# Kernel optimization log

Hardware: AMD Instinct MI355X
Metric: run time of the kernel (lower is better)

Reference implementation:

```python
import jax, jax.numpy as jnp
import numpy as np

N = 100000
E = 1600000
NFEAT = 256
NHID = 128
LATENT = 64


def setup_inputs() -> dict:
    key = jax.random.key(0)
    ks = jax.random.split(key, 12)
    x = jax.random.normal(ks[0], (N, NFEAT), dtype=jnp.float32)
    edge_index = jax.random.randint(ks[1], (2, E), 0, N, dtype=jnp.int32)
    edge_weight = jax.random.uniform(ks[2], (E,), dtype=jnp.float32)
    # GraphConvolution params: uniform(-stdv, stdv), stdv = 1/sqrt(out_features)
    s1 = 1.0 / np.sqrt(NHID)
    gc1_w = jax.random.uniform(ks[3], (NFEAT, NHID), minval=-s1, maxval=s1, dtype=jnp.float32)
    gc1_b = jax.random.uniform(ks[4], (NHID,), minval=-s1, maxval=s1, dtype=jnp.float32)
    gc2_w = jax.random.uniform(ks[5], (NHID, NHID), minval=-s1, maxval=s1, dtype=jnp.float32)
    gc2_b = jax.random.uniform(ks[6], (NHID,), minval=-s1, maxval=s1, dtype=jnp.float32)
    # nn.Linear default init: uniform(-1/sqrt(fan_in), 1/sqrt(fan_in))
    s2 = 1.0 / np.sqrt(NHID)
    mu_w = jax.random.uniform(ks[7], (NHID, LATENT), minval=-s2, maxval=s2, dtype=jnp.float32)
    mu_b = jax.random.uniform(ks[8], (LATENT,), minval=-s2, maxval=s2, dtype=jnp.float32)
    lv_w = jax.random.uniform(ks[9], (NHID, LATENT), minval=-s2, maxval=s2, dtype=jnp.float32)
    lv_b = jax.random.uniform(ks[10], (LATENT,), minval=-s2, maxval=s2, dtype=jnp.float32)
    return {"x": x, "edge_index": edge_index, "edge_weight": edge_weight,
            "gc1_w": gc1_w, "gc1_b": gc1_b, "gc2_w": gc2_w, "gc2_b": gc2_b,
            "mu_w": mu_w, "mu_b": mu_b, "lv_w": lv_w, "lv_b": lv_b}


def _spmm(edge_index, edge_weight, support):
    # out[row] += w * support[col]  (sparse adj @ dense support)
    row, col = edge_index[0], edge_index[1]
    msgs = support[col] * edge_weight[:, None]          # [E, F]
    return jax.ops.segment_sum(msgs, row, num_segments=N)


def reference(x, edge_index, edge_weight, gc1_w, gc1_b, gc2_w, gc2_b,
              mu_w, mu_b, lv_w, lv_b):
    # gc1: mm -> spmm -> bias -> relu (dropout is identity in eval mode)
    h = jax.nn.relu(_spmm(edge_index, edge_weight, x @ gc1_w) + gc1_b)
    h = jax.nn.relu(_spmm(edge_index, edge_weight, h @ gc2_w) + gc2_b)
    mu = h @ mu_w + mu_b
    log_var = h @ lv_w + lv_b
    return mu, log_var
```

## Files before the change

### kernel.cpp

```cpp
#include <hip/hip_runtime.h>
#include <hip/hip_fp16.h>

#define N_NODES 100000
#define N_EDGES 1600000
#define NFEAT   256
#define NHID    128
#define LATENT  64

#define NBUCKET 782
#define NBLKH   196
#define CHUNK   8192
#define NHIST   (NBUCKET * NBLKH)
#define NROWT   196
#define NHISTT  300

typedef __attribute__((ext_vector_type(8))) short s16x8;
typedef __attribute__((ext_vector_type(4))) float f32x4;

__device__ __forceinline__ unsigned short f2bf(float f) {
    union { float f; unsigned u; } v; v.f = f;
    unsigned r = v.u + 0x7fffu + ((v.u >> 16) & 1u);
    return (unsigned short)(r >> 16);
}
__device__ __forceinline__ float bf2f(unsigned short s) {
    union { unsigned u; float f; } v; v.u = ((unsigned)s) << 16;
    return v.f;
}
__device__ __forceinline__ float w15_decode(unsigned pv) {
    return __half2float(__ushort_as_half((unsigned short)(pv & 0x7fffu)));
}

__device__ __forceinline__ int incl_scan512(int v, int t, int (&s)[2][512]) {
    s[0][t] = v;
    __syncthreads();
    int p = 0;
    for (int off = 1; off < 512; off <<= 1) {
        int x = s[p][t];
        if (t >= off) x += s[p][t - off];
        s[p ^ 1][t] = x;
        p ^= 1;
        __syncthreads();
    }
    return s[p][t];
}


__device__ __forceinline__ void prep_body(
    int c, int K, int Ntot, int ncol0, int ldb0, int ldb1,
    const float* __restrict__ B0, const float* __restrict__ B1,
    unsigned short* __restrict__ out)
{
    int K8 = K >> 3;
    int total = (Ntot >> 4) * K8 * 16;
    if (c >= total) return;
    int m  = c & 15;
    int kc = (c >> 4) % K8;
    int nt = (c >> 4) / K8;
    int col = nt * 16 + m;
    const float* src; int ld, cc;
    if (col < ncol0) { src = B0; ld = ldb0; cc = col; }
    else             { src = B1; ld = ldb1; cc = col - ncol0; }
    s16x8 v;
    #pragma unroll
    for (int j = 0; j < 8; ++j)
        v[j] = (short)f2bf(src[(size_t)(kc * 8 + j) * ld + cc]);
    *(s16x8*)&out[(size_t)c * 8] = v;
}


__global__ __launch_bounds__(256) void k_pre(
    const int* __restrict__ rows, int* __restrict__ deg,
    int* __restrict__ histG,
    const float* __restrict__ gc1_w, unsigned short* __restrict__ w1p,
    const float* __restrict__ gc2_w, unsigned short* __restrict__ w2p,
    const float* __restrict__ mu_w, const float* __restrict__ lv_w,
    unsigned short* __restrict__ w3p)
{
    int b = blockIdx.x;
    int t = threadIdx.x;
    if (b < NBLKH) {
        __shared__ int hist[NBUCKET];
        for (int i = t; i < NBUCKET; i += 256) hist[i] = 0;
        __syncthreads();
        int base = b * CHUNK;
        #pragma unroll 4
        for (int i = 0; i < CHUNK / 256; ++i) {
            int e = base + i * 256 + t;
            if (e < N_EDGES) {
                int r = rows[e];
                atomicAdd(&deg[r], 1);
                atomicAdd(&hist[r >> 7], 1);
            }
        }
        __syncthreads();
        for (int i = t; i < NBUCKET; i += 256)
            histG[(size_t)i * NBLKH + b] = hist[i];
    } else if (b < NBLKH + 16) {
        prep_body((b - NBLKH) * 256 + t, NFEAT, NHID, NHID, NHID, NHID, gc1_w, gc1_w, w1p);
    } else if (b < NBLKH + 24) {
        prep_body((b - NBLKH - 16) * 256 + t, NHID, NHID, NHID, NHID, NHID, gc2_w, gc2_w, w2p);
    } else {
        prep_body((b - NBLKH - 24) * 256 + t, NHID, NHID, LATENT, LATENT, LATENT, mu_w, lv_w, w3p);
    }
}


__global__ __launch_bounds__(512) void k_scanA(
    const int* __restrict__ deg, int* __restrict__ row_excl, int* __restrict__ rbsum,
    const int* __restrict__ histG, int* __restrict__ hist_excl, int* __restrict__ hbsum)
{
    __shared__ int s[2][512];
    int b = blockIdx.x, t = threadIdx.x;
    if (b < NROWT) {
        int i = b * 512 + t;
        int v = (i < N_NODES) ? deg[i] : 0;
        int incl = incl_scan512(v, t, s);
        if (i < N_NODES) row_excl[i] = incl - v;
        if (t == 511) rbsum[b] = incl;
    } else {
        int bb = b - NROWT;
        int i = bb * 512 + t;
        int v = (i < NHIST) ? histG[i] : 0;
        int incl = incl_scan512(v, t, s);
        if (i < NHIST) hist_excl[i] = incl - v;
        if (t == 511) hbsum[bb] = incl;
    }
}

__global__ __launch_bounds__(512) void k_scanB(int* __restrict__ rbsum,
                                               int* __restrict__ hbsum)
{
    __shared__ int s[2][512];
    int t = threadIdx.x;
    int* arr = (blockIdx.x == 0) ? rbsum : hbsum;
    int n    = (blockIdx.x == 0) ? NROWT : NHISTT;
    int v = (t < n) ? arr[t] : 0;
    int incl = incl_scan512(v, t, s);
    if (t < n) arr[t] = incl - v;
}

__global__ __launch_bounds__(512) void k_scanC(
    const int* __restrict__ row_excl, const int* __restrict__ rbsum,
    int* __restrict__ row_ptr,
    const int* __restrict__ hist_excl, const int* __restrict__ hbsum,
    int* __restrict__ scanned)
{
    int b = blockIdx.x, t = threadIdx.x;
    if (b < NROWT) {
        int i = b * 512 + t;
        if (i < N_NODES) row_ptr[i] = row_excl[i] + rbsum[b];
        if (b == 0 && t == 0) row_ptr[N_NODES] = N_EDGES;
    } else {
        int bb = b - NROWT;
        int i = bb * 512 + t;
        if (i < NHIST) scanned[i] = hist_excl[i] + hbsum[bb];
    }
}


__global__ __launch_bounds__(256) void k_scatterA(
    const int* __restrict__ rows, const int* __restrict__ cols,
    const float* __restrict__ ew, const int* __restrict__ scanned,
    uint2* __restrict__ tmp)
{
    __shared__ int cur[NBUCKET];
    int b = blockIdx.x, t = threadIdx.x;
    for (int i = t; i < NBUCKET; i += 256)
        cur[i] = scanned[(size_t)i * NBLKH + b];
    __syncthreads();
    int base = b * CHUNK;
    #pragma unroll 4
    for (int i = 0; i < CHUNK / 256; ++i) {
        int e = base + i * 256 + t;
        if (e < N_EDGES) {
            int r = rows[e];
            unsigned hv = (unsigned)__half_as_ushort(__float2half(ew[e]));
            unsigned pv = ((unsigned)cols[e] << 15) | (hv & 0x7fffu);
            int p = atomicAdd(&cur[r >> 7], 1);
            tmp[p] = make_uint2(pv, (unsigned)r);
        }
    }
}


__global__ __launch_bounds__(256) void k_passB(
    const int* __restrict__ row_ptr, const uint2* __restrict__ tmp,
    unsigned* __restrict__ ecw)
{
    __shared__ int cur[128];
    int b  = blockIdx.x;
    int r0 = b * 128;
    int t  = threadIdx.x;
    if (t < 128) {
        int rr = r0 + t;
        cur[t] = (rr < N_NODES) ? row_ptr[rr] : N_EDGES;
    }
    __syncthreads();
    int beg = row_ptr[r0];
    int rend = r0 + 128; if (rend > N_NODES) rend = N_NODES;
    int end = row_ptr[rend];
    for (int e = beg + t; e < end; e += 256) {
        uint2 v = tmp[e];
        int p = atomicAdd(&cur[v.y & 127], 1);
        ecw[p] = v.x;
    }
}


template<int AMODE, int OMODE>
__global__ __launch_bounds__(256) void k_gemm(
    int K, const float* __restrict__ A32, const unsigned short* __restrict__ A16,
    const unsigned short* __restrict__ Bpre,
    unsigned short* __restrict__ C16,
    float* __restrict__ C0, float* __restrict__ C1,
    const float* __restrict__ bias0, const float* __restrict__ bias1)
{
    __shared__ unsigned short As[2048];
    __shared__ unsigned short Bs[8192];

    const int t    = threadIdx.x;
    const int m0   = blockIdx.x * 32;
    const int lane = t & 63;
    const int w    = t >> 6;
    const int rt   = w & 1;
    const int ntb  = (w >> 1) * 4;
    const int fm   = lane & 15;
    const int q    = lane >> 4;
    const int K8   = K >> 3;

    f32x4 acc[4] = {};

    for (int kt = 0; kt < K; kt += 64) {
        {
            int r = t >> 3, kc = t & 7;
            int lo = ((r >> 4) * 8 + kc) * 128 + (r & 15) * 8;
            if (AMODE == 0) {
                const float* g = A32 + (size_t)(m0 + r) * K + kt + kc * 8;
                float4 a = *(const float4*)g;
                float4 b = *(const float4*)(g + 4);
                s16x8 v;
                v[0] = (short)f2bf(a.x); v[1] = (short)f2bf(a.y);
                v[2] = (short)f2bf(a.z); v[3] = (short)f2bf(a.w);
                v[4] = (short)f2bf(b.x); v[5] = (short)f2bf(b.y);
                v[6] = (short)f2bf(b.z); v[7] = (short)f2bf(b.w);
                *(s16x8*)&As[lo] = v;
            } else {
                const unsigned short* g = A16 + (size_t)(m0 + r) * 128 + kt + kc * 8;
                *(s16x8*)&As[lo] = *(const s16x8*)g;
            }
        }
        {
            int ktc = kt >> 3;
            #pragma unroll
            for (int i = 0; i < 4; ++i) {
                int c  = t + i * 256;
                int nt = c >> 7, kc = (c >> 4) & 7, m = c & 15;
                const unsigned short* g =
                    Bpre + ((size_t)(nt * K8 + ktc + kc) * 16 + m) * 8;
                *(s16x8*)&Bs[c * 8] = *(const s16x8*)g;
            }
        }
        __syncthreads();
        #pragma unroll
        for (int kk = 0; kk < 2; ++kk) {
            int kcq = kk * 4 + q;
            s16x8 a = *(const s16x8*)&As[(rt * 8 + kcq) * 128 + fm * 8];
            #pragma unroll
            for (int i = 0; i < 4; ++i) {
                s16x8 b = *(const s16x8*)&Bs[((ntb + i) * 8 + kcq) * 128 + fm * 8];
                acc[i] = __builtin_amdgcn_mfma_f32_16x16x32_bf16(a, b, acc[i], 0, 0, 0);
            }
        }
        __syncthreads();
    }

    #pragma unroll
    for (int i = 0; i < 4; ++i) {
        int col = (ntb + i) * 16 + fm;
        #pragma unroll
        for (int j = 0; j < 4; ++j) {
            int r = m0 + rt * 16 + q * 4 + j;
            float v = acc[i][j];
            if (OMODE == 0) {
                C16[(size_t)r * 128 + col] = f2bf(v);
            } else {
                if (col < 64) C0[(size_t)r * 64 + col]      = v + bias0[col];
                else          C1[(size_t)r * 64 + col - 64] = v + bias1[col - 64];
            }
        }
    }
}


__global__ __launch_bounds__(256) void k_spmm(const int* __restrict__ row_ptr,
                                              const unsigned* __restrict__ ecw,
                                              const unsigned short* __restrict__ sup,
                                              const float* __restrict__ bias,
                                              unsigned short* __restrict__ out) {
    int wave = threadIdx.x >> 6;
    int lane = threadIdx.x & 63;
    int row  = blockIdx.x * 4 + wave;
    if (row >= N_NODES) return;
    int half = lane >> 5;
    int fl   = lane & 31;

    int beg = row_ptr[row];
    int end = row_ptr[row + 1];
    float a0 = 0.f, a1 = 0.f, a2 = 0.f, a3 = 0.f;

    int n8 = beg + ((end - beg) & ~7);
    for (int e = beg; e < n8; e += 8) {
        unsigned q0 = ecw[e + 0 + half];
        unsigned q1 = ecw[e + 2 + half];
        unsigned q2 = ecw[e + 4 + half];
        unsigned q3 = ecw[e + 6 + half];
        uint2 v0 = *(const uint2*)(sup + (size_t)(q0 >> 15) * NHID + fl * 4);
        uint2 v1 = *(const uint2*)(sup + (size_t)(q1 >> 15) * NHID + fl * 4);
        uint2 v2 = *(const uint2*)(sup + (size_t)(q2 >> 15) * NHID + fl * 4);
        uint2 v3 = *(const uint2*)(sup + (size_t)(q3 >> 15) * NHID + fl * 4);
        float w0 = w15_decode(q0), w1 = w15_decode(q1);
        float w2 = w15_decode(q2), w3 = w15_decode(q3);
        a0 += w0 * bf2f((unsigned short)v0.x);
        a1 += w0 * bf2f((unsigned short)(v0.x >> 16));
        a2 += w0 * bf2f((unsigned short)v0.y);
        a3 += w0 * bf2f((unsigned short)(v0.y >> 16));
        a0 += w1 * bf2f((unsigned short)v1.x);
        a1 += w1 * bf2f((unsigned short)(v1.x >> 16));
        a2 += w1 * bf2f((unsigned short)v1.y);
        a3 += w1 * bf2f((unsigned short)(v1.y >> 16));
        a0 += w2 * bf2f((unsigned short)v2.x);
        a1 += w2 * bf2f((unsigned short)(v2.x >> 16));
        a2 += w2 * bf2f((unsigned short)v2.y);
        a3 += w2 * bf2f((unsigned short)(v2.y >> 16));
        a0 += w3 * bf2f((unsigned short)v3.x);
        a1 += w3 * bf2f((unsigned short)(v3.x >> 16));
        a2 += w3 * bf2f((unsigned short)v3.y);
        a3 += w3 * bf2f((unsigned short)(v3.y >> 16));
    }
    for (int e = n8; e < end; e += 2) {
        int ee = e + half;
        if (ee < end) {
            unsigned q = ecw[ee];
            uint2 v = *(const uint2*)(sup + (size_t)(q >> 15) * NHID + fl * 4);
            float w = w15_decode(q);
            a0 += w * bf2f((unsigned short)v.x);
            a1 += w * bf2f((unsigned short)(v.x >> 16));
            a2 += w * bf2f((unsigned short)v.y);
            a3 += w * bf2f((unsigned short)(v.y >> 16));
        }
    }
    a0 += __shfl_xor(a0, 32, 64);
    a1 += __shfl_xor(a1, 32, 64);
    a2 += __shfl_xor(a2, 32, 64);
    a3 += __shfl_xor(a3, 32, 64);

    if (half == 0) {
        float o0 = a0 + bias[fl * 4 + 0];
        float o1 = a1 + bias[fl * 4 + 1];
        float o2 = a2 + bias[fl * 4 + 2];
        float o3 = a3 + bias[fl * 4 + 3];
        o0 = o0 > 0.f ? o0 : 0.f;
        o1 = o1 > 0.f ? o1 : 0.f;
        o2 = o2 > 0.f ? o2 : 0.f;
        o3 = o3 > 0.f ? o3 : 0.f;
        uint2 pv;
        pv.x = (unsigned)f2bf(o0) | ((unsigned)f2bf(o1) << 16);
        pv.y = (unsigned)f2bf(o2) | ((unsigned)f2bf(o3) << 16);
        *(uint2*)(out + (size_t)row * NHID + fl * 4) = pv;
    }
}


extern "C" void kernel_launch(void* const* d_in, const int* in_sizes, int n_in,
                              void* d_out, int out_size, void* d_ws, size_t ws_size,
                              hipStream_t stream) {
    const float* x     = (const float*)d_in[0];
    const int*   ei    = (const int*)  d_in[1];
    const float* ew    = (const float*)d_in[2];
    const float* gc1_w = (const float*)d_in[3];
    const float* gc1_b = (const float*)d_in[4];
    const float* gc2_w = (const float*)d_in[5];
    const float* gc2_b = (const float*)d_in[6];
    const float* mu_w  = (const float*)d_in[7];
    const float* mu_b  = (const float*)d_in[8];
    const float* lv_w  = (const float*)d_in[9];
    const float* lv_b  = (const float*)d_in[10];
    float* out = (float*)d_out;

    const int* rows = ei;
    const int* cols = ei + N_EDGES;

    char* p = (char*)d_ws;
    auto alloc = [&](size_t bytes) {
        char* r = p;
        p += (bytes + 255) & ~(size_t)255;
        return r;
    };
    int*      deg       = (int*)     alloc((size_t)N_NODES * 4);
    int*      row_excl  = (int*)     alloc((size_t)N_NODES * 4);
    int*      row_ptr   = (int*)     alloc((size_t)(N_NODES + 1) * 4);
    int*      rbsum     = (int*)     alloc((size_t)NROWT * 4);
    int*      histG     = (int*)     alloc((size_t)NHIST * 4);
    int*      hist_excl = (int*)     alloc((size_t)NHIST * 4);
    int*      hbsum     = (int*)     alloc((size_t)NHISTT * 4);
    int*      scanned   = (int*)     alloc((size_t)NHIST * 4);
    unsigned* ecw       = (unsigned*)alloc((size_t)N_EDGES * 4);
    uint2*    tmp       = (uint2*)   alloc((size_t)N_EDGES * 8);
    unsigned short* w1p    = (unsigned short*)alloc((size_t)NFEAT * NHID * 2);
    unsigned short* w2p    = (unsigned short*)alloc((size_t)NHID * NHID * 2);
    unsigned short* w3p    = (unsigned short*)alloc((size_t)NHID * NHID * 2);
    unsigned short* bufSup = (unsigned short*)alloc((size_t)N_NODES * NHID * 2);
    unsigned short* bufH   = (unsigned short*)alloc((size_t)N_NODES * NHID * 2);
    (void)ws_size; (void)n_in; (void)in_sizes; (void)out_size;

    hipMemsetAsync(deg, 0, (size_t)N_NODES * 4, stream);
    k_pre<<<NBLKH + 32, 256, 0, stream>>>(rows, deg, histG,
                                          gc1_w, w1p, gc2_w, w2p, mu_w, lv_w, w3p);
    k_scanA<<<NROWT + NHISTT, 512, 0, stream>>>(deg, row_excl, rbsum,
                                                histG, hist_excl, hbsum);
    k_scanB<<<2, 512, 0, stream>>>(rbsum, hbsum);
    k_scanC<<<NROWT + NHISTT, 512, 0, stream>>>(row_excl, rbsum, row_ptr,
                                                hist_excl, hbsum, scanned);
    k_scatterA<<<NBLKH, 256, 0, stream>>>(rows, cols, ew, scanned, tmp);
    k_passB<<<NBUCKET, 256, 0, stream>>>(row_ptr, tmp, ecw);

    k_gemm<0, 0><<<N_NODES / 32, 256, 0, stream>>>(NFEAT, x, nullptr, w1p,
                                                   bufSup, nullptr, nullptr, nullptr, nullptr);
    k_spmm<<<N_NODES / 4, 256, 0, stream>>>(row_ptr, ecw, bufSup, gc1_b, bufH);
    k_gemm<1, 0><<<N_NODES / 32, 256, 0, stream>>>(NHID, nullptr, bufH, w2p,
                                                   bufSup, nullptr, nullptr, nullptr, nullptr);
    k_spmm<<<N_NODES / 4, 256, 0, stream>>>(row_ptr, ecw, bufSup, gc2_b, bufH);
    k_gemm<1, 1><<<N_NODES / 32, 256, 0, stream>>>(NHID, nullptr, bufH, w3p,
                                                   nullptr, out, out + (size_t)N_NODES * LATENT,
                                                   mu_b, lv_b);
}
```

Measured before the change: 487.9 us.

## Derive row_ptr inside bucket pass, dropping global degree atomics and scans

Removes the per-edge global atomic degree count, the degree memset, and the node-level multi-kernel scan. row_ptr is now computed inside k_passB from a per-bucket local histogram and a shared-memory scan, offset by the bucket's start in the already-scanned histogram. The small block-sum scan (k_scanB) is folded into k_scanC, where every block redundantly rescans the 300 block sums. This saves one global atomic per edge and several launches, at the cost of an extra read pass over tmp in k_passB.

After: 435.2 us. 1.12x faster.

```diff
diff --git a/kernel.cpp b/kernel.cpp
--- a/kernel.cpp
+++ b/kernel.cpp
@@ -11,7 +11,6 @@
 #define NBLKH   196
 #define CHUNK   8192
 #define NHIST   (NBUCKET * NBLKH)
-#define NROWT   196
 #define NHISTT  300
 
 typedef __attribute__((ext_vector_type(8))) short s16x8;
@@ -69,8 +68,7 @@
 
 
 __global__ __launch_bounds__(256) void k_pre(
-    const int* __restrict__ rows, int* __restrict__ deg,
-    int* __restrict__ histG,
+    const int* __restrict__ rows, int* __restrict__ histG,
     const float* __restrict__ gc1_w, unsigned short* __restrict__ w1p,
     const float* __restrict__ gc2_w, unsigned short* __restrict__ w2p,
     const float* __restrict__ mu_w, const float* __restrict__ lv_w,
@@ -88,7 +86,6 @@
             int e = base + i * 256 + t;
             if (e < N_EDGES) {
                 int r = rows[e];
-                atomicAdd(&deg[r], 1);
                 atomicAdd(&hist[r >> 7], 1);
             }
         }
@@ -106,55 +103,32 @@
 
 
 __global__ __launch_bounds__(512) void k_scanA(
-    const int* __restrict__ deg, int* __restrict__ row_excl, int* __restrict__ rbsum,
-    const int* __restrict__ histG, int* __restrict__ hist_excl, int* __restrict__ hbsum)
+    const int* __restrict__ histG, int* __restrict__ hist_excl,
+    int* __restrict__ hbsum)
 {
     __shared__ int s[2][512];
     int b = blockIdx.x, t = threadIdx.x;
-    if (b < NROWT) {
-        int i = b * 512 + t;
-        int v = (i < N_NODES) ? deg[i] : 0;
-        int incl = incl_scan512(v, t, s);
-        if (i < N_NODES) row_excl[i] = incl - v;
-        if (t == 511) rbsum[b] = incl;
-    } else {
-        int bb = b - NROWT;
-        int i = bb * 512 + t;
-        int v = (i < NHIST) ? histG[i] : 0;
-        int incl = incl_scan512(v, t, s);
-        if (i < NHIST) hist_excl[i] = incl - v;
-        if (t == 511) hbsum[bb] = incl;
-    }
-}
-
-__global__ __launch_bounds__(512) void k_scanB(int* __restrict__ rbsum,
-                                               int* __restrict__ hbsum)
-{
-    __shared__ int s[2][512];
-    int t = threadIdx.x;
-    int* arr = (blockIdx.x == 0) ? rbsum : hbsum;
-    int n    = (blockIdx.x == 0) ? NROWT : NHISTT;
-    int v = (t < n) ? arr[t] : 0;
+    int i = b * 512 + t;
+    int v = (i < NHIST) ? histG[i] : 0;
     int incl = incl_scan512(v, t, s);
-    if (t < n) arr[t] = incl - v;
+    if (i < NHIST) hist_excl[i] = incl - v;
+    if (t == 511) hbsum[b] = incl;
 }
 
 __global__ __launch_bounds__(512) void k_scanC(
-    const int* __restrict__ row_excl, const int* __restrict__ rbsum,
-    int* __restrict__ row_ptr,
     const int* __restrict__ hist_excl, const int* __restrict__ hbsum,
     int* __restrict__ scanned)
 {
+    __shared__ int s[2][512];
+    __shared__ int sbase;
     int b = blockIdx.x, t = threadIdx.x;
-    if (b < NROWT) {
-        int i = b * 512 + t;
-        if (i < N_NODES) row_ptr[i] = row_excl[i] + rbsum[b];
-        if (b == 0 && t == 0) row_ptr[N_NODES] = N_EDGES;
-    } else {
-        int bb = b - NROWT;
-        int i = bb * 512 + t;
-        if (i < NHIST) scanned[i] = hist_excl[i] + hbsum[bb];
-    }
+    int v = (t < NHISTT) ? hbsum[t] : 0;
+    int incl = incl_scan512(v, t, s);
+    if (t == b) sbase = incl - v;
+    __syncthreads();
+    int base = sbase;
+    int i = b * 512 + t;
+    if (i < NHIST) scanned[i] = hist_excl[i] + base;
 }
 
 
@@ -184,25 +158,46 @@
 
 
 __global__ __launch_bounds__(256) void k_passB(
-    const int* __restrict__ row_ptr, const uint2* __restrict__ tmp,
-    unsigned* __restrict__ ecw)
-{
+    const int* __restrict__ scanned, const uint2* __restrict__ tmp,
+    unsigned* __restrict__ ecw, int* __restrict__ row_ptr)
+{
+    __shared__ int cnt[128];
+    __shared__ int sc[2][128];
     __shared__ int cur[128];
     int b  = blockIdx.x;
+    int t  = threadIdx.x;
     int r0 = b * 128;
-    int t  = threadIdx.x;
+    int beg = scanned[(size_t)b * NBLKH];
+    int end = (b + 1 < NBUCKET) ? scanned[(size_t)(b + 1) * NBLKH] : N_EDGES;
+    if (t < 128) cnt[t] = 0;
+    __syncthreads();
+    for (int e = beg + t; e < end; e += 256)
+        atomicAdd(&cnt[tmp[e].y & 127], 1);
+    __syncthreads();
+    int p = 0;
+    if (t < 128) sc[0][t] = cnt[t];
+    __syncthreads();
+    for (int off = 1; off < 128; off <<= 1) {
+        if (t < 128) {
+            int x = sc[p][t];
+            if (t >= off) x += sc[p][t - off];
+            sc[p ^ 1][t] = x;
+        }
+        p ^= 1;
+        __syncthreads();
+    }
     if (t < 128) {
+        int excl = sc[p][t] - cnt[t];
         int rr = r0 + t;
-        cur[t] = (rr < N_NODES) ? row_ptr[rr] : N_EDGES;
-    }
-    __syncthreads();
-    int beg = row_ptr[r0];
-    int rend = r0 + 128; if (rend > N_NODES) rend = N_NODES;
-    int end = row_ptr[rend];
+        if (rr < N_NODES) row_ptr[rr] = beg + excl;
+        cur[t] = beg + excl;
+    }
+    if (b == NBUCKET - 1 && t == 0) row_ptr[N_NODES] = N_EDGES;
+    __syncthreads();
     for (int e = beg + t; e < end; e += 256) {
         uint2 v = tmp[e];
-        int p = atomicAdd(&cur[v.y & 127], 1);
-        ecw[p] = v.x;
+        int pos = atomicAdd(&cur[v.y & 127], 1);
+        ecw[pos] = v.x;
     }
 }
 
@@ -396,10 +391,7 @@
         p += (bytes + 255) & ~(size_t)255;
         return r;
     };
-    int*      deg       = (int*)     alloc((size_t)N_NODES * 4);
-    int*      row_excl  = (int*)     alloc((size_t)N_NODES * 4);
     int*      row_ptr   = (int*)     alloc((size_t)(N_NODES + 1) * 4);
-    int*      rbsum     = (int*)     alloc((size_t)NROWT * 4);
     int*      histG     = (int*)     alloc((size_t)NHIST * 4);
     int*      hist_excl = (int*)     alloc((size_t)NHIST * 4);
     int*      hbsum     = (int*)     alloc((size_t)NHISTT * 4);
@@ -413,16 +405,12 @@
     unsigned short* bufH   = (unsigned short*)alloc((size_t)N_NODES * NHID * 2);
     (void)ws_size; (void)n_in; (void)in_sizes; (void)out_size;
 
-    hipMemsetAsync(deg, 0, (size_t)N_NODES * 4, stream);
-    k_pre<<<NBLKH + 32, 256, 0, stream>>>(rows, deg, histG,
+    k_pre<<<NBLKH + 32, 256, 0, stream>>>(rows, histG,
                                           gc1_w, w1p, gc2_w, w2p, mu_w, lv_w, w3p);
-    k_scanA<<<NROWT + NHISTT, 512, 0, stream>>>(deg, row_excl, rbsum,
-                                                histG, hist_excl, hbsum);
-    k_scanB<<<2, 512, 0, stream>>>(rbsum, hbsum);
-    k_scanC<<<NROWT + NHISTT, 512, 0, stream>>>(row_excl, rbsum, row_ptr,
-                                                hist_excl, hbsum, scanned);
+    k_scanA<<<NHISTT, 512, 0, stream>>>(histG, hist_excl, hbsum);
+    k_scanC<<<NHISTT, 512, 0, stream>>>(hist_excl, hbsum, scanned);
     k_scatterA<<<NBLKH, 256, 0, stream>>>(rows, cols, ew, scanned, tmp);
-    k_passB<<<NBUCKET, 256, 0, stream>>>(row_ptr, tmp, ecw);
+    k_passB<<<NBUCKET, 256, 0, stream>>>(scanned, tmp, ecw, row_ptr);
 
     k_gemm<0, 0><<<N_NODES / 32, 256, 0, stream>>>(NFEAT, x, nullptr, w1p,
                                                    bufSup, nullptr, nullptr, nullptr, nullptr);
```
